# Kernel tuning notes

Hardware: AMD Instinct MI355X
Metric: run time of the kernel (lower is better)

## Reference

```python
import jax, jax.numpy as jnp
import numpy as np

DIM = 512
HEADS = 8
DIM_HEAD = 64
SCALE = DIM_HEAD ** -0.5


def setup_inputs() -> dict:
    key = jax.random.key(0)
    ks = jax.random.split(key, 4)
    b, n = 4, 2048
    x = jax.random.normal(ks[0], (b, n, DIM), dtype=jnp.float32)
    Wq = jax.random.normal(ks[1], (DIM, HEADS * DIM_HEAD), dtype=jnp.float32) * (DIM ** -0.5)
    Wkv = jax.random.normal(ks[2], (DIM, 2 * HEADS * DIM_HEAD), dtype=jnp.float32) * (DIM ** -0.5)
    Wo = jax.random.normal(ks[3], (HEADS * DIM_HEAD, DIM), dtype=jnp.float32) * ((HEADS * DIM_HEAD) ** -0.5)
    bo = jnp.zeros((DIM,), dtype=jnp.float32)
    return {"x": x, "Wq": Wq, "Wkv": Wkv, "Wo": Wo, "bo": bo}


def reference(x, Wq, Wkv, Wo, bo):
    b, n, _ = x.shape
    # context = x (self-attention path, kv_include_self=False)
    q = x @ Wq                      # [b, n, h*d]
    kv = x @ Wkv                    # [b, n, 2*h*d]
    k, v = jnp.split(kv, 2, axis=-1)

    def split_heads(t):
        return t.reshape(b, n, HEADS, DIM_HEAD).transpose(0, 2, 1, 3)  # [b,h,n,d]

    q, k, v = split_heads(q), split_heads(k), split_heads(v)
    dots = jnp.einsum('bhid,bhjd->bhij', q, k) * SCALE  # [b,h,n,n]
    attn = jax.nn.softmax(dots, axis=-1)
    out = jnp.einsum('bhij,bhjd->bhid', attn, v)        # [b,h,n,d]
    out = out.transpose(0, 2, 1, 3).reshape(b, n, HEADS * DIM_HEAD)
    return out @ Wo + bo
```

## Files before the change

kernel.cpp:

```cpp
#include <hip/hip_runtime.h>
#include <hip/hip_bf16.h>

typedef short bf16x8 __attribute__((ext_vector_type(8)));
typedef float fx4    __attribute__((ext_vector_type(4)));
typedef unsigned uint32x2 __attribute__((ext_vector_type(2)));

#if __has_builtin(__builtin_amdgcn_exp2f)
#define EXP2 __builtin_amdgcn_exp2f
#else
#define EXP2 exp2f
#endif

__device__ __forceinline__ unsigned pk2(float a, float b) {
  union { __hip_bfloat162 h; unsigned u; } cv;
  cv.h = __float22bfloat162_rn(float2{a, b});
  return cv.u;
}
__device__ __forceinline__ uint2 pk4(const fx4& v) {
  uint2 r;
  r.x = pk2(v[0], v[1]);
  r.y = pk2(v[2], v[3]);
  return r;
}

__device__ __forceinline__ void gld16(const void* g, void* l) {
  __builtin_amdgcn_global_load_lds(
      (const __attribute__((address_space(1))) unsigned int*)g,
      (__attribute__((address_space(3))) unsigned int*)l, 16, 0, 0);
}

__device__ __forceinline__ void bar_raw() {
  asm volatile("s_barrier" ::: "memory");
}
__device__ __forceinline__ void bar_lgkm() {
  asm volatile("s_waitcnt lgkmcnt(0)\ns_barrier" ::: "memory");
}
__device__ __forceinline__ void bar_lgkm_vm8() {
  asm volatile("s_waitcnt vmcnt(8) lgkmcnt(0)\ns_barrier" ::: "memory");
}
__device__ __forceinline__ void bar_vm_lgkm() {
  asm volatile("s_waitcnt vmcnt(0) lgkmcnt(0)\ns_barrier" ::: "memory");
}
__device__ __forceinline__ void cfence() { asm volatile("" ::: "memory"); }

__global__ __launch_bounds__(256) void prep_kernel(
    const float* __restrict__ x, const float* __restrict__ Wq,
    const float* __restrict__ Wkv, const float* __restrict__ Wo,
    short* __restrict__ xb, short* __restrict__ WallT, short* __restrict__ WoT,
    float qscale) {
  const int bx = blockIdx.x, tid = threadIdx.x;
  if (bx < 4096) {
    int i = bx * 256 + tid;
    const float4 s = *(const float4*)(x + (size_t)i * 4);
    uint2 o; o.x = pk2(s.x, s.y); o.y = pk2(s.z, s.w);
    *(uint2*)(xb + (size_t)i * 4) = o;
    return;
  }
  __shared__ float t[32][33];
  const int idx = bx - 4096;
  const int wb = idx & 63, kt = (idx >> 6) * 32;
  const bool mode0 = wb < 48;
  const int ct = (mode0 ? wb : wb - 48) * 32;
  const int tx = tid & 31, ty = tid >> 5;
  short* outT = mode0 ? WallT : WoT;
#pragma unroll
  for (int s = 0; s < 4; ++s) {
    int k = kt + ty + s * 8;
    int c = ct + tx;
    float v;
    if (mode0) v = (c < 512) ? Wq[(size_t)k * 512 + c] * qscale
                             : Wkv[(size_t)k * 1024 + (c - 512)];
    else       v = Wo[(size_t)k * 512 + c];
    t[ty + s * 8][tx] = v;
  }
  __syncthreads();
#pragma unroll
  for (int s = 0; s < 4; ++s) {
    int c = ct + ty + s * 8;
    int k = kt + tx;
    unsigned u = __float_as_uint(t[tx][ty + s * 8]);
    u = (u + 0x7fffu + ((u >> 16) & 1u)) >> 16;
    outT[(size_t)c * 512 + k] = (short)u;
  }
}

__global__ __launch_bounds__(256) void gemm_qkv(
    const short* __restrict__ A, const short* __restrict__ Bt,
    short* __restrict__ oq, short* __restrict__ ok, short* __restrict__ ovT) {
  __shared__ __align__(16) char smem[49152];
  short* As  = (short*)smem;
  short* BsA = (short*)(smem + 16384);
  short* BsB = (short*)(smem + 32768);
  short* T   = (short*)smem;
  const int K = 512;
  const int tid = threadIdx.x;
  const int wave = tid >> 6, lane = tid & 63;
  const int quad = lane >> 4, l15 = lane & 15;
  const int wm = wave >> 1, wn = wave & 1;
  const int blk = blockIdx.x;
  const int xcd = blk & 7, slot = blk >> 3;
  const int m0 = ((slot / 12) * 8 + xcd) * 128;
  const int n0 = (slot % 12) * 128;
  const bool swapped = (n0 < 1024);

  int arow[4], aoff[4];
#pragma unroll
  for (int c = 0; c < 4; ++c) {
    int u = c * 256 + tid;
    int slab = u >> 9, r2 = u & 511;
    arow[c] = r2 >> 2;
    aoff[c] = slab * 32 + (r2 & 3) * 8;
  }

  fx4 acc[4][4];
#pragma unroll
  for (int i = 0; i < 4; ++i)
#pragma unroll
    for (int j = 0; j < 4; ++j) acc[i][j] = fx4{0.f, 0.f, 0.f, 0.f};

  auto BDMA = [&](int k0, short* Bc) {
#pragma unroll
    for (int c = 0; c < 4; ++c) {
      int u = c * 256 + tid;
      int slab = u >> 9, r2 = u & 511;
      gld16(Bt + (size_t)(n0 + (r2 >> 2)) * K + k0 + slab * 32 + (r2 & 3) * 8,
            Bc + (size_t)(c * 256 + wave * 64) * 8);
    }
  };

  auto COMPUTE = [&](const short* Bc) {
#pragma unroll
    for (int ks2 = 0; ks2 < 2; ++ks2) {
      bf16x8 af[4], bfr[4];
#pragma unroll
      for (int i = 0; i < 4; ++i)
        af[i] = *(const bf16x8*)(As + ks2 * 4096 + (wm * 64 + i * 16 + l15) * 32 + quad * 8);
#pragma unroll
      for (int i = 0; i < 4; ++i)
        bfr[i] = *(const bf16x8*)(Bc + ks2 * 4096 + (wn * 64 + i * 16 + l15) * 32 + quad * 8);
      if (swapped) {
#pragma unroll
        for (int mi = 0; mi < 4; ++mi)
#pragma unroll
          for (int ni = 0; ni < 4; ++ni)
            acc[mi][ni] = __builtin_amdgcn_mfma_f32_16x16x32_bf16(bfr[ni], af[mi], acc[mi][ni], 0, 0, 0);
      } else {
#pragma unroll
        for (int mi = 0; mi < 4; ++mi)
#pragma unroll
          for (int ni = 0; ni < 4; ++ni)
            acc[mi][ni] = __builtin_amdgcn_mfma_f32_16x16x32_bf16(af[mi], bfr[ni], acc[mi][ni], 0, 0, 0);
      }
    }
  };

  BDMA(0, BsA);
  cfence();
  bf16x8 apre[4];
#pragma unroll
  for (int c = 0; c < 4; ++c)
    apre[c] = *(const bf16x8*)(A + (size_t)(m0 + arow[c]) * K + aoff[c]);

  for (int t = 0; t < 7; ++t) {
    bar_raw();
#pragma unroll
    for (int c = 0; c < 4; ++c)
      *(bf16x8*)(As + (size_t)(c * 256 + tid) * 8) = apre[c];
    BDMA((t + 1) * 64, ((t + 1) & 1) ? BsB : BsA);
    cfence();
    {
      int kn = (t + 1) * 64;
#pragma unroll
      for (int c = 0; c < 4; ++c)
        apre[c] = *(const bf16x8*)(A + (size_t)(m0 + arow[c]) * K + kn + aoff[c]);
    }
    bar_lgkm_vm8();
    COMPUTE((t & 1) ? BsB : BsA);
  }
  bar_raw();
#pragma unroll
  for (int c = 0; c < 4; ++c)
    *(bf16x8*)(As + (size_t)(c * 256 + tid) * 8) = apre[c];
  bar_lgkm();
  COMPUTE(BsB);

  const int cls = n0 >> 9;
  const int fbase = n0 & 511;
  const int bb = m0 >> 11;
  const int iib = m0 & 2047;

  bar_lgkm();
  if (cls < 2) {
#pragma unroll
    for (int mi = 0; mi < 4; ++mi) {
      int bl_m = wm * 64 + mi * 16 + l15;
#pragma unroll
      for (int ni = 0; ni < 4; ++ni) {
        int bl_c = wn * 64 + ni * 16 + quad * 4;
        *(uint2*)(T + bl_m * 136 + bl_c) = pk4(acc[mi][ni]);
      }
    }
    bar_lgkm();
    short* base = (cls == 0) ? oq : ok;
#pragma unroll
    for (int p = 0; p < 8; ++p) {
      int u = p * 256 + tid;
      int row = u >> 4, c0 = (u & 15) * 8;
      int f = fbase + c0;
      int hh = f >> 6, dd = f & 63;
      uint4 v = *(const uint4*)(T + row * 136 + c0);
      *(uint4*)(base + ((size_t)(bb * 8 + hh) * 2048 + iib + row) * 64 + dd) = v;
    }
  } else {
#pragma unroll
    for (int mi = 0; mi < 4; ++mi) {
      int bl_m = wm * 64 + mi * 16 + quad * 4;
#pragma unroll
      for (int ni = 0; ni < 4; ++ni) {
        int bl_c = wn * 64 + ni * 16 + l15;
        *(uint2*)(T + bl_c * 136 + bl_m) = pk4(acc[mi][ni]);
      }
    }
    bar_lgkm();
#pragma unroll
    for (int p = 0; p < 8; ++p) {
      int u = p * 256 + tid;
      int c = u >> 4, m8 = (u & 15) * 8;
      int f = fbase + c;
      int hh = f >> 6, dd = f & 63;
      uint4 v = *(const uint4*)(T + c * 136 + m8);
      *(uint4*)(ovT + ((size_t)(bb * 8 + hh) * 64 + dd) * 2048 + iib + m8) = v;
    }
  }
}

__global__ __launch_bounds__(256) void gemm_out(
    const short* __restrict__ A, const short* __restrict__ Bt,
    float* __restrict__ of, const float* __restrict__ bias) {
  __shared__ short As[2 * 64 * 32];
  __shared__ short Bs[2 * 128 * 32];
  const int K = 512, N = 512;
  const int tid = threadIdx.x;
  const int wave = tid >> 6, lane = tid & 63;
  const int quad = lane >> 4, l15 = lane & 15;
  const int wm = wave >> 1, wn = wave & 1;
  const int m0 = blockIdx.y * 64, n0 = blockIdx.x * 128;

  int arow[2], aoff[2], brow[4], boff[4];
#pragma unroll
  for (int c = 0; c < 2; ++c) {
    int u = c * 256 + tid;
    int slab = u >> 8, r2 = u & 255;
    arow[c] = r2 >> 2; aoff[c] = slab * 32 + (r2 & 3) * 8;
  }
#pragma unroll
  for (int c = 0; c < 4; ++c) {
    int u = c * 256 + tid;
    int slab = u >> 9, r2 = u & 511;
    brow[c] = r2 >> 2; boff[c] = slab * 32 + (r2 & 3) * 8;
  }

  fx4 acc[2][4];
#pragma unroll
  for (int i = 0; i < 2; ++i)
#pragma unroll
    for (int j = 0; j < 4; ++j) acc[i][j] = fx4{0.f, 0.f, 0.f, 0.f};

  bf16x8 apre[2], bpre[4];
#pragma unroll
  for (int c = 0; c < 2; ++c)
    apre[c] = *(const bf16x8*)(A + (size_t)(m0 + arow[c]) * K + aoff[c]);
#pragma unroll
  for (int c = 0; c < 4; ++c)
    bpre[c] = *(const bf16x8*)(Bt + (size_t)(n0 + brow[c]) * K + boff[c]);

  for (int k0 = 0; k0 < K; k0 += 64) {
    bar_raw();
#pragma unroll
    for (int c = 0; c < 2; ++c)
      *(bf16x8*)(As + (size_t)(c * 256 + tid) * 8) = apre[c];
#pragma unroll
    for (int c = 0; c < 4; ++c)
      *(bf16x8*)(Bs + (size_t)(c * 256 + tid) * 8) = bpre[c];
    {
      int kn = (k0 + 64) & 511;
#pragma unroll
      for (int c = 0; c < 2; ++c)
        apre[c] = *(const bf16x8*)(A + (size_t)(m0 + arow[c]) * K + kn + aoff[c]);
#pragma unroll
      for (int c = 0; c < 4; ++c)
        bpre[c] = *(const bf16x8*)(Bt + (size_t)(n0 + brow[c]) * K + kn + boff[c]);
    }
    bar_lgkm();

#pragma unroll
    for (int ks2 = 0; ks2 < 2; ++ks2) {
      bf16x8 af[2], bfr[4];
#pragma unroll
      for (int i = 0; i < 2; ++i)
        af[i] = *(const bf16x8*)(As + ks2 * 2048 + (wm * 32 + i * 16 + l15) * 32 + quad * 8);
#pragma unroll
      for (int i = 0; i < 4; ++i)
        bfr[i] = *(const bf16x8*)(Bs + ks2 * 4096 + (wn * 64 + i * 16 + l15) * 32 + quad * 8);
#pragma unroll
      for (int mi = 0; mi < 2; ++mi)
#pragma unroll
        for (int ni = 0; ni < 4; ++ni)
          acc[mi][ni] = __builtin_amdgcn_mfma_f32_16x16x32_bf16(af[mi], bfr[ni], acc[mi][ni], 0, 0, 0);
    }
  }

  const int rowb = m0 + wm * 32;
  const int colb = n0 + wn * 64;
#pragma unroll
  for (int mi = 0; mi < 2; ++mi)
#pragma unroll
    for (int ni = 0; ni < 4; ++ni) {
      int cg = colb + ni * 16 + l15;
      float bv = bias[cg];
#pragma unroll
      for (int r = 0; r < 4; ++r) {
        int rg = rowb + mi * 16 + quad * 4 + r;
        of[(size_t)rg * N + cg] = acc[mi][ni][r] + bv;
      }
    }
}

__global__ __launch_bounds__(256, 2) void attn_kernel(
    const short* __restrict__ Q, const short* __restrict__ K,
    const short* __restrict__ Vt, short* __restrict__ O) {
  __shared__ short Ks[2 * 64 * 64];
  __shared__ short Vs[2 * 64 * 64];

  const int tid = threadIdx.x;
  const int wave = tid >> 6, lane = tid & 63;
  const int quad = lane >> 4, l15 = lane & 15;
  const int blk = blockIdx.x;
  const int xcd = blk & 7, slot = blk >> 3;
  const int bh = (slot >> 4) * 8 + xcd;
  const int qt = slot & 15;
  const int b = bh >> 3, h = bh & 7;
  const int i0 = qt * 128 + wave * 32;

  const int idx0 = tid, idx1 = 256 + tid;
  const int row0 = idx0 >> 3, sg0 = (idx0 & 7) ^ (row0 & 7);
  const int row1 = idx1 >> 3, sg1 = (idx1 & 7) ^ (row1 & 7);
  const short* Kb = K + (size_t)bh * 2048 * 64;
  const short* Vb = Vt + (size_t)bh * 64 * 2048;

  bf16x8 qf[2][2];
#pragma unroll
  for (int it = 0; it < 2; ++it)
#pragma unroll
    for (int ks = 0; ks < 2; ++ks)
      qf[it][ks] = *(const bf16x8*)(Q + ((size_t)bh * 2048 + i0 + it * 16 + l15) * 64 + ks * 32 + quad * 8);

  bf16x8 ones;
#pragma unroll
  for (int c = 0; c < 8; ++c) ones[c] = (short)0x3F80;

  fx4 oacc[2][4];
  fx4 acc_l[2] = { fx4{0.f,0.f,0.f,0.f}, fx4{0.f,0.f,0.f,0.f} };
#pragma unroll
  for (int it = 0; it < 2; ++it)
#pragma unroll
    for (int dt = 0; dt < 4; ++dt) oacc[it][dt] = fx4{0.f, 0.f, 0.f, 0.f};

  auto DMA = [&](int jn, int bufsel) {
    const int nb = bufsel * 4096;
    gld16(Kb + (size_t)(jn + row0) * 64 + sg0 * 8, Ks + nb + wave * 512);
    gld16(Kb + (size_t)(jn + row1) * 64 + sg1 * 8, Ks + nb + 2048 + wave * 512);
    gld16(Vb + (size_t)row0 * 2048 + jn + sg0 * 8, Vs + nb + wave * 512);
    gld16(Vb + (size_t)row1 * 2048 + jn + sg1 * 8, Vs + nb + 2048 + wave * 512);
  };

  auto QK = [&](const short* Kc, fx4 (&s)[2][4]) {
#pragma unroll
    for (int it = 0; it < 2; ++it)
#pragma unroll
      for (int jt = 0; jt < 4; ++jt) s[it][jt] = fx4{0.f, 0.f, 0.f, 0.f};
#pragma unroll
    for (int ks = 0; ks < 2; ++ks) {
#pragma unroll
      for (int jt = 0; jt < 4; ++jt) {
        bf16x8 kf = *(const bf16x8*)(Kc + (jt * 16 + l15) * 64 + (((ks * 4 + quad) ^ (l15 & 7)) * 8));
#pragma unroll
        for (int it = 0; it < 2; ++it)
          s[it][jt] = __builtin_amdgcn_mfma_f32_16x16x32_bf16(kf, qf[it][ks], s[it][jt], 0, 0, 0);
      }
    }
  };

  auto VLOAD = [&](const short* Vc, bf16x8 (&vf)[2][4]) {
#pragma unroll
    for (int kj = 0; kj < 2; ++kj)
#pragma unroll
      for (int dt = 0; dt < 4; ++dt)
        vf[kj][dt] = *(const bf16x8*)(Vc + (dt * 16 + l15) * 64 + (((kj * 4 + quad) ^ (l15 & 7)) * 8));
  };

  auto SMPV = [&](fx4 (&s)[2][4], bf16x8 (&vf)[2][4]) {
#pragma unroll
    for (int it = 0; it < 2; ++it) {
      unsigned W[4][2];
#pragma unroll
      for (int jt = 0; jt < 4; ++jt) {
#pragma unroll
        for (int r = 0; r < 4; ++r) s[it][jt][r] = EXP2(s[it][jt][r]);
        W[jt][0] = pk2(s[it][jt][0], s[it][jt][1]);
        W[jt][1] = pk2(s[it][jt][2], s[it][jt][3]);
      }
#pragma unroll
      for (int k = 0; k < 2; ++k) {
        union { unsigned u[4]; bf16x8 v; } pw;
#pragma unroll
        for (int hh = 0; hh < 2; ++hh) {
          uint32x2 a = __builtin_amdgcn_permlane32_swap(W[2 * k][hh], W[2 * k + 1][hh], false, false);
          uint32x2 t = __builtin_amdgcn_permlane16_swap(a[0], a[1], false, false);
          pw.u[hh] = t[0];
          pw.u[2 + hh] = t[1];
        }
        acc_l[it] = __builtin_amdgcn_mfma_f32_16x16x32_bf16(ones, pw.v, acc_l[it], 0, 0, 0);
#pragma unroll
        for (int dt = 0; dt < 4; ++dt)
          oacc[it][dt] = __builtin_amdgcn_mfma_f32_16x16x32_bf16(vf[k][dt], pw.v, oacc[it][dt], 0, 0, 0);
      }
    }
  };

  fx4 sA[2][4], sB[2][4];
  bf16x8 vfA[2][4], vfB[2][4];

  DMA(0, 0);
  bar_vm_lgkm();
  DMA(64, 1);
  QK(Ks, sA);
  VLOAD(Vs, vfA);

  for (int t1 = 1; t1 <= 29; t1 += 2) {
    bar_vm_lgkm();
    DMA((t1 + 1) << 6, 0);
    QK(Ks + 4096, sB);
    VLOAD(Vs + 4096, vfB);
    SMPV(sA, vfA);
    bar_vm_lgkm();
    DMA((t1 + 2) << 6, 1);
    QK(Ks, sA);
    VLOAD(Vs, vfA);
    SMPV(sB, vfB);
  }

  bar_vm_lgkm();
  QK(Ks + 4096, sB);
  VLOAD(Vs + 4096, vfB);
  SMPV(sA, vfA);
  SMPV(sB, vfB);

#pragma unroll
  for (int it = 0; it < 2; ++it) {
    float inv = __builtin_amdgcn_rcpf(acc_l[it][0]);
    size_t rowbase = ((size_t)b * 2048 + i0 + it * 16 + l15) * 512 + h * 64;
#pragma unroll
    for (int dt = 0; dt < 4; ++dt) {
      fx4 o = oacc[it][dt] * inv;
      *(uint2*)(O + rowbase + dt * 16 + quad * 4) = pk4(o);
    }
  }
}

extern "C" void kernel_launch(void* const* d_in, const int* in_sizes, int n_in,
                              void* d_out, int out_size, void* d_ws, size_t ws_size,
                              hipStream_t stream) {
  const float* x   = (const float*)d_in[0];
  const float* Wq  = (const float*)d_in[1];
  const float* Wkv = (const float*)d_in[2];
  const float* Wo  = (const float*)d_in[3];
  const float* bo  = (const float*)d_in[4];
  float* out = (float*)d_out;

  char* p = (char*)d_ws;
  short* xb    = (short*)p; p += (size_t)8192 * 512 * 2;
  short* WallT = (short*)p; p += (size_t)1536 * 512 * 2;
  short* WoT   = (short*)p; p += (size_t)512 * 512 * 2;
  short* qb    = (short*)p; p += (size_t)32 * 2048 * 64 * 2;
  short* kb    = (short*)p; p += (size_t)32 * 2048 * 64 * 2;
  short* vTb   = (short*)p; p += (size_t)32 * 64 * 2048 * 2;
  short* Ob    = (short*)p; p += (size_t)8192 * 512 * 2;

  const float qscale = 0.125f * 1.4426950408889634f;

  prep_kernel<<<5120, 256, 0, stream>>>(x, Wq, Wkv, Wo, xb, WallT, WoT, qscale);
  gemm_qkv<<<768, 256, 0, stream>>>(xb, WallT, qb, kb, vTb);
  attn_kernel<<<512, 256, 0, stream>>>(qb, kb, vTb, Ob);
  gemm_out<<<dim3(4, 128), 256, 0, stream>>>(Ob, WoT, out, bo);
}
```

Before: 151.5 us.

## Merge four kernels into two cooperative launches with grid-wide sync

Wraps the prep, QKV GEMM, attention and output GEMM bodies as device functions and fuses them pairwise into two cooperative kernels separated by grid.sync, with a fallback to the original four launches if the cooperative launch fails. The goal is to remove kernel launch gaps and tail effects between stages. In exchange it adds grid-barrier cost and system-scope fences, caps occupancy because the whole grid must be co-resident, and the prep stage now loops over virtual blocks within 768 resident blocks.

```diff
diff --git a/kernel.cpp b/kernel.cpp
--- a/kernel.cpp
+++ b/kernel.cpp
@@ -1,5 +1,8 @@
 #include <hip/hip_runtime.h>
+#include <hip/hip_cooperative_groups.h>
 #include <hip/hip_bf16.h>
+
+namespace cg = cooperative_groups;
 
 typedef short bf16x8 __attribute__((ext_vector_type(8)));
 typedef float fx4    __attribute__((ext_vector_type(4)));
@@ -43,26 +46,28 @@
 }
 __device__ __forceinline__ void cfence() { asm volatile("" ::: "memory"); }
 
-__global__ __launch_bounds__(256) void prep_kernel(
+
+__device__ __forceinline__ void prep_body(
+    int vb, int tid, void* smem,
     const float* __restrict__ x, const float* __restrict__ Wq,
     const float* __restrict__ Wkv, const float* __restrict__ Wo,
     short* __restrict__ xb, short* __restrict__ WallT, short* __restrict__ WoT,
     float qscale) {
-  const int bx = blockIdx.x, tid = threadIdx.x;
-  if (bx < 4096) {
-    int i = bx * 256 + tid;
+  if (vb < 4096) {
+    int i = vb * 256 + tid;
     const float4 s = *(const float4*)(x + (size_t)i * 4);
     uint2 o; o.x = pk2(s.x, s.y); o.y = pk2(s.z, s.w);
     *(uint2*)(xb + (size_t)i * 4) = o;
     return;
   }
-  __shared__ float t[32][33];
-  const int idx = bx - 4096;
+  float (*t)[33] = (float(*)[33])smem;
+  const int idx = vb - 4096;
   const int wb = idx & 63, kt = (idx >> 6) * 32;
   const bool mode0 = wb < 48;
   const int ct = (mode0 ? wb : wb - 48) * 32;
   const int tx = tid & 31, ty = tid >> 5;
   short* outT = mode0 ? WallT : WoT;
+  __syncthreads();
 #pragma unroll
   for (int s = 0; s < 4; ++s) {
     int k = kt + ty + s * 8;
@@ -84,20 +89,18 @@
   }
 }
 
-__global__ __launch_bounds__(256) void gemm_qkv(
+__device__ __forceinline__ void qkv_body(
+    int blk, int tid, char* smem,
     const short* __restrict__ A, const short* __restrict__ Bt,
     short* __restrict__ oq, short* __restrict__ ok, short* __restrict__ ovT) {
-  __shared__ __align__(16) char smem[49152];
   short* As  = (short*)smem;
   short* BsA = (short*)(smem + 16384);
   short* BsB = (short*)(smem + 32768);
   short* T   = (short*)smem;
   const int K = 512;
-  const int tid = threadIdx.x;
   const int wave = tid >> 6, lane = tid & 63;
   const int quad = lane >> 4, l15 = lane & 15;
   const int wm = wave >> 1, wn = wave & 1;
-  const int blk = blockIdx.x;
   const int xcd = blk & 7, slot = blk >> 3;
   const int m0 = ((slot / 12) * 8 + xcd) * 128;
   const int n0 = (slot % 12) * 128;
@@ -234,108 +237,14 @@
   }
 }
 
-__global__ __launch_bounds__(256) void gemm_out(
-    const short* __restrict__ A, const short* __restrict__ Bt,
-    float* __restrict__ of, const float* __restrict__ bias) {
-  __shared__ short As[2 * 64 * 32];
-  __shared__ short Bs[2 * 128 * 32];
-  const int K = 512, N = 512;
-  const int tid = threadIdx.x;
+__device__ __forceinline__ void attn_body(
+    int blk, int tid, char* smem,
+    const short* __restrict__ Q, const short* __restrict__ Kq,
+    const short* __restrict__ Vt, short* __restrict__ O) {
+  short* Ks = (short*)smem;
+  short* Vs = (short*)(smem + 16384);
   const int wave = tid >> 6, lane = tid & 63;
   const int quad = lane >> 4, l15 = lane & 15;
-  const int wm = wave >> 1, wn = wave & 1;
-  const int m0 = blockIdx.y * 64, n0 = blockIdx.x * 128;
-
-  int arow[2], aoff[2], brow[4], boff[4];
-#pragma unroll
-  for (int c = 0; c < 2; ++c) {
-    int u = c * 256 + tid;
-    int slab = u >> 8, r2 = u & 255;
-    arow[c] = r2 >> 2; aoff[c] = slab * 32 + (r2 & 3) * 8;
-  }
-#pragma unroll
-  for (int c = 0; c < 4; ++c) {
-    int u = c * 256 + tid;
-    int slab = u >> 9, r2 = u & 511;
-    brow[c] = r2 >> 2; boff[c] = slab * 32 + (r2 & 3) * 8;
-  }
-
-  fx4 acc[2][4];
-#pragma unroll
-  for (int i = 0; i < 2; ++i)
-#pragma unroll
-    for (int j = 0; j < 4; ++j) acc[i][j] = fx4{0.f, 0.f, 0.f, 0.f};
-
-  bf16x8 apre[2], bpre[4];
-#pragma unroll
-  for (int c = 0; c < 2; ++c)
-    apre[c] = *(const bf16x8*)(A + (size_t)(m0 + arow[c]) * K + aoff[c]);
-#pragma unroll
-  for (int c = 0; c < 4; ++c)
-    bpre[c] = *(const bf16x8*)(Bt + (size_t)(n0 + brow[c]) * K + boff[c]);
-
-  for (int k0 = 0; k0 < K; k0 += 64) {
-    bar_raw();
-#pragma unroll
-    for (int c = 0; c < 2; ++c)
-      *(bf16x8*)(As + (size_t)(c * 256 + tid) * 8) = apre[c];
-#pragma unroll
-    for (int c = 0; c < 4; ++c)
-      *(bf16x8*)(Bs + (size_t)(c * 256 + tid) * 8) = bpre[c];
-    {
-      int kn = (k0 + 64) & 511;
-#pragma unroll
-      for (int c = 0; c < 2; ++c)
-        apre[c] = *(const bf16x8*)(A + (size_t)(m0 + arow[c]) * K + kn + aoff[c]);
-#pragma unroll
-      for (int c = 0; c < 4; ++c)
-        bpre[c] = *(const bf16x8*)(Bt + (size_t)(n0 + brow[c]) * K + kn + boff[c]);
-    }
-    bar_lgkm();
-
-#pragma unroll
-    for (int ks2 = 0; ks2 < 2; ++ks2) {
-      bf16x8 af[2], bfr[4];
-#pragma unroll
-      for (int i = 0; i < 2; ++i)
-        af[i] = *(const bf16x8*)(As + ks2 * 2048 + (wm * 32 + i * 16 + l15) * 32 + quad * 8);
-#pragma unroll
-      for (int i = 0; i < 4; ++i)
-        bfr[i] = *(const bf16x8*)(Bs + ks2 * 4096 + (wn * 64 + i * 16 + l15) * 32 + quad * 8);
-#pragma unroll
-      for (int mi = 0; mi < 2; ++mi)
-#pragma unroll
-        for (int ni = 0; ni < 4; ++ni)
-          acc[mi][ni] = __builtin_amdgcn_mfma_f32_16x16x32_bf16(af[mi], bfr[ni], acc[mi][ni], 0, 0, 0);
-    }
-  }
-
-  const int rowb = m0 + wm * 32;
-  const int colb = n0 + wn * 64;
-#pragma unroll
-  for (int mi = 0; mi < 2; ++mi)
-#pragma unroll
-    for (int ni = 0; ni < 4; ++ni) {
-      int cg = colb + ni * 16 + l15;
-      float bv = bias[cg];
-#pragma unroll
-      for (int r = 0; r < 4; ++r) {
-        int rg = rowb + mi * 16 + quad * 4 + r;
-        of[(size_t)rg * N + cg] = acc[mi][ni][r] + bv;
-      }
-    }
-}
-
-__global__ __launch_bounds__(256, 2) void attn_kernel(
-    const short* __restrict__ Q, const short* __restrict__ K,
-    const short* __restrict__ Vt, short* __restrict__ O) {
-  __shared__ short Ks[2 * 64 * 64];
-  __shared__ short Vs[2 * 64 * 64];
-
-  const int tid = threadIdx.x;
-  const int wave = tid >> 6, lane = tid & 63;
-  const int quad = lane >> 4, l15 = lane & 15;
-  const int blk = blockIdx.x;
   const int xcd = blk & 7, slot = blk >> 3;
   const int bh = (slot >> 4) * 8 + xcd;
   const int qt = slot & 15;
@@ -345,7 +254,7 @@
   const int idx0 = tid, idx1 = 256 + tid;
   const int row0 = idx0 >> 3, sg0 = (idx0 & 7) ^ (row0 & 7);
   const int row1 = idx1 >> 3, sg1 = (idx1 & 7) ^ (row1 & 7);
-  const short* Kb = K + (size_t)bh * 2048 * 64;
+  const short* Kb = Kq + (size_t)bh * 2048 * 64;
   const short* Vb = Vt + (size_t)bh * 64 * 2048;
 
   bf16x8 qf[2][2];
@@ -468,6 +377,160 @@
   }
 }
 
+__device__ __forceinline__ void out_body(
+    int vb, int tid, char* smem,
+    const short* __restrict__ A, const short* __restrict__ Bt,
+    float* __restrict__ of, const float* __restrict__ bias) {
+  short* As = (short*)smem;
+  short* Bs = (short*)(smem + 8192);
+  const int K = 512, N = 512;
+  const int wave = tid >> 6, lane = tid & 63;
+  const int quad = lane >> 4, l15 = lane & 15;
+  const int wm = wave >> 1, wn = wave & 1;
+  const int n0 = (vb & 3) * 128, m0 = (vb >> 2) * 64;
+
+  int arow[2], aoff[2], brow[4], boff[4];
+#pragma unroll
+  for (int c = 0; c < 2; ++c) {
+    int u = c * 256 + tid;
+    int slab = u >> 8, r2 = u & 255;
+    arow[c] = r2 >> 2; aoff[c] = slab * 32 + (r2 & 3) * 8;
+  }
+#pragma unroll
+  for (int c = 0; c < 4; ++c) {
+    int u = c * 256 + tid;
+    int slab = u >> 9, r2 = u & 511;
+    brow[c] = r2 >> 2; boff[c] = slab * 32 + (r2 & 3) * 8;
+  }
+
+  fx4 acc[2][4];
+#pragma unroll
+  for (int i = 0; i < 2; ++i)
+#pragma unroll
+    for (int j = 0; j < 4; ++j) acc[i][j] = fx4{0.f, 0.f, 0.f, 0.f};
+
+  bf16x8 apre[2], bpre[4];
+#pragma unroll
+  for (int c = 0; c < 2; ++c)
+    apre[c] = *(const bf16x8*)(A + (size_t)(m0 + arow[c]) * K + aoff[c]);
+#pragma unroll
+  for (int c = 0; c < 4; ++c)
+    bpre[c] = *(const bf16x8*)(Bt + (size_t)(n0 + brow[c]) * K + boff[c]);
+
+  for (int k0 = 0; k0 < K; k0 += 64) {
+    bar_raw();
+#pragma unroll
+    for (int c = 0; c < 2; ++c)
+      *(bf16x8*)(As + (size_t)(c * 256 + tid) * 8) = apre[c];
+#pragma unroll
+    for (int c = 0; c < 4; ++c)
+      *(bf16x8*)(Bs + (size_t)(c * 256 + tid) * 8) = bpre[c];
+    {
+      int kn = (k0 + 64) & 511;
+#pragma unroll
+      for (int c = 0; c < 2; ++c)
+        apre[c] = *(const bf16x8*)(A + (size_t)(m0 + arow[c]) * K + kn + aoff[c]);
+#pragma unroll
+      for (int c = 0; c < 4; ++c)
+        bpre[c] = *(const bf16x8*)(Bt + (size_t)(n0 + brow[c]) * K + kn + boff[c]);
+    }
+    bar_lgkm();
+
+#pragma unroll
+    for (int ks2 = 0; ks2 < 2; ++ks2) {
+      bf16x8 af[2], bfr[4];
+#pragma unroll
+      for (int i = 0; i < 2; ++i)
+        af[i] = *(const bf16x8*)(As + ks2 * 2048 + (wm * 32 + i * 16 + l15) * 32 + quad * 8);
+#pragma unroll
+      for (int i = 0; i < 4; ++i)
+        bfr[i] = *(const bf16x8*)(Bs + ks2 * 4096 + (wn * 64 + i * 16 + l15) * 32 + quad * 8);
+#pragma unroll
+      for (int mi = 0; mi < 2; ++mi)
+#pragma unroll
+        for (int ni = 0; ni < 4; ++ni)
+          acc[mi][ni] = __builtin_amdgcn_mfma_f32_16x16x32_bf16(af[mi], bfr[ni], acc[mi][ni], 0, 0, 0);
+    }
+  }
+
+  const int rowb = m0 + wm * 32;
+  const int colb = n0 + wn * 64;
+#pragma unroll
+  for (int mi = 0; mi < 2; ++mi)
+#pragma unroll
+    for (int ni = 0; ni < 4; ++ni) {
+      int cg_ = colb + ni * 16 + l15;
+      float bv = bias[cg_];
+#pragma unroll
+      for (int r = 0; r < 4; ++r) {
+        int rg = rowb + mi * 16 + quad * 4 + r;
+        of[(size_t)rg * N + cg_] = acc[mi][ni][r] + bv;
+      }
+    }
+}
+
+
+__global__ __launch_bounds__(256) void prep_kernel(
+    const float* __restrict__ x, const float* __restrict__ Wq,
+    const float* __restrict__ Wkv, const float* __restrict__ Wo,
+    short* __restrict__ xb, short* __restrict__ WallT, short* __restrict__ WoT,
+    float qscale) {
+  __shared__ float t[32][33];
+  prep_body(blockIdx.x, threadIdx.x, (void*)t, x, Wq, Wkv, Wo, xb, WallT, WoT, qscale);
+}
+
+__global__ __launch_bounds__(256) void gemm_qkv(
+    const short* __restrict__ A, const short* __restrict__ Bt,
+    short* __restrict__ oq, short* __restrict__ ok, short* __restrict__ ovT) {
+  __shared__ __align__(16) char smem[49152];
+  qkv_body(blockIdx.x, threadIdx.x, smem, A, Bt, oq, ok, ovT);
+}
+
+__global__ __launch_bounds__(256, 2) void attn_kernel(
+    const short* __restrict__ Q, const short* __restrict__ Kq,
+    const short* __restrict__ Vt, short* __restrict__ O) {
+  __shared__ __align__(16) char smem[32768];
+  attn_body(blockIdx.x, threadIdx.x, smem, Q, Kq, Vt, O);
+}
+
+__global__ __launch_bounds__(256) void gemm_out(
+    const short* __restrict__ A, const short* __restrict__ Bt,
+    float* __restrict__ of, const float* __restrict__ bias) {
+  __shared__ __align__(16) char smem[24576];
+  out_body(blockIdx.y * 4 + blockIdx.x, threadIdx.x, smem, A, Bt, of, bias);
+}
+
+
+__global__ __launch_bounds__(256, 3) void k_prep_qkv(
+    const float* __restrict__ x, const float* __restrict__ Wq,
+    const float* __restrict__ Wkv, const float* __restrict__ Wo,
+    short* __restrict__ xb, short* __restrict__ WallT, short* __restrict__ WoT,
+    float qscale,
+    short* __restrict__ oq, short* __restrict__ ok, short* __restrict__ ovT) {
+  __shared__ __align__(16) char smem[49152];
+  const int tid = threadIdx.x;
+  for (int vb = blockIdx.x; vb < 5120; vb += 768)
+    prep_body(vb, tid, (void*)smem, x, Wq, Wkv, Wo, xb, WallT, WoT, qscale);
+  __threadfence_system();
+  cg::this_grid().sync();
+  __threadfence_system();
+  qkv_body(blockIdx.x, tid, smem, xb, WallT, oq, ok, ovT);
+}
+
+__global__ __launch_bounds__(256, 2) void k_attn_out(
+    const short* __restrict__ Q, const short* __restrict__ Kq,
+    const short* __restrict__ Vt, short* __restrict__ O,
+    const short* __restrict__ WoT, float* __restrict__ of,
+    const float* __restrict__ bias) {
+  __shared__ __align__(16) char smem[32768];
+  const int tid = threadIdx.x;
+  attn_body(blockIdx.x, tid, smem, Q, Kq, Vt, O);
+  __threadfence_system();
+  cg::this_grid().sync();
+  __threadfence_system();
+  out_body(blockIdx.x, tid, smem, O, WoT, of, bias);
+}
+
 extern "C" void kernel_launch(void* const* d_in, const int* in_sizes, int n_in,
                               void* d_out, int out_size, void* d_ws, size_t ws_size,
                               hipStream_t stream) {
@@ -487,10 +550,36 @@
   short* vTb   = (short*)p; p += (size_t)32 * 64 * 2048 * 2;
   short* Ob    = (short*)p; p += (size_t)8192 * 512 * 2;
 
-  const float qscale = 0.125f * 1.4426950408889634f;
-
-  prep_kernel<<<5120, 256, 0, stream>>>(x, Wq, Wkv, Wo, xb, WallT, WoT, qscale);
-  gemm_qkv<<<768, 256, 0, stream>>>(xb, WallT, qb, kb, vTb);
-  attn_kernel<<<512, 256, 0, stream>>>(qb, kb, vTb, Ob);
-  gemm_out<<<dim3(4, 128), 256, 0, stream>>>(Ob, WoT, out, bo);
-}
+  float qscale = 0.125f * 1.4426950408889634f;
+
+  static bool coop_ok = true;
+
+  bool k1_coop = false;
+  if (coop_ok) {
+    void* a1[] = { (void*)&x, (void*)&Wq, (void*)&Wkv, (void*)&Wo,
+                   (void*)&xb, (void*)&WallT, (void*)&WoT, (void*)&qscale,
+                   (void*)&qb, (void*)&kb, (void*)&vTb };
+    hipError_t e = hipLaunchCooperativeKernel((const void*)k_prep_qkv,
+                                              dim3(768), dim3(256), a1, 0, stream);
+    if (e == hipSuccess) k1_coop = true;
+    else coop_ok = false;
+  }
+  if (!k1_coop) {
+    prep_kernel<<<5120, 256, 0, stream>>>(x, Wq, Wkv, Wo, xb, WallT, WoT, qscale);
+    gemm_qkv<<<768, 256, 0, stream>>>(xb, WallT, qb, kb, vTb);
+  }
+
+  bool k2_coop = false;
+  if (coop_ok) {
+    void* a2[] = { (void*)&qb, (void*)&kb, (void*)&vTb, (void*)&Ob,
+                   (void*)&WoT, (void*)&out, (void*)&bo };
+    hipError_t e = hipLaunchCooperativeKernel((const void*)k_attn_out,
+                                              dim3(512), dim3(256), a2, 0, stream);
+    if (e == hipSuccess) k2_coop = true;
+    else coop_ok = false;
+  }
+  if (!k2_coop) {
+    attn_kernel<<<512, 256, 0, stream>>>(qb, kb, vTb, Ob);
+    gemm_out<<<dim3(4, 128), 256, 0, stream>>>(Ob, WoT, out, bo);
+  }
+}
```

Result: no change. 150.9 us (-0.4%).
